# Optimization experiments

Hardware: AMD Instinct MI355X
Metric: run time of the kernel (lower is better)

## Reference

```python
import jax, jax.numpy as jnp
import numpy as np

N_HEAD, D_EMB, D_MLP, D_HEAD = 12, 768, 3072, 64
LN_EPS = 1e-5


def setup_inputs() -> dict:
    key = jax.random.key(0)
    ks = jax.random.split(key, 12)
    s = 0.02
    return {
        "x": jax.random.normal(ks[0], (2, 4096, D_EMB), dtype=jnp.float32),
        "ln1_g": jnp.ones((D_EMB,), jnp.float32),
        "ln1_b": jnp.zeros((D_EMB,), jnp.float32),
        "wqkv_w": jax.random.normal(ks[1], (D_EMB, 3 * D_EMB), jnp.float32) * s,
        "wo_w": jax.random.normal(ks[2], (D_EMB, D_EMB), jnp.float32) * s,
        "wo_b": jnp.zeros((D_EMB,), jnp.float32),
        "ln2_g": jnp.ones((D_EMB,), jnp.float32),
        "ln2_b": jnp.zeros((D_EMB,), jnp.float32),
        "w1_w": jax.random.normal(ks[3], (D_EMB, D_MLP), jnp.float32) * s,
        "w1_b": jnp.zeros((D_MLP,), jnp.float32),
        "w2_w": jax.random.normal(ks[4], (D_MLP, D_EMB), jnp.float32) * s,
        "w2_b": jnp.zeros((D_EMB,), jnp.float32),
    }


def _layernorm(x, g, b):
    mu = jnp.mean(x, axis=-1, keepdims=True)
    var = jnp.var(x, axis=-1, keepdims=True)
    return (x - mu) * jax.lax.rsqrt(var + LN_EPS) * g + b


def _attn(x, wqkv_w, wo_w, wo_b):
    B, T, d = x.shape
    qkv = x @ wqkv_w  # [B,T,3d]
    q, k, v = jnp.split(qkv, 3, axis=-1)
    q = q.reshape(B, T, N_HEAD, D_HEAD).transpose(0, 2, 1, 3)  # [B,H,T,dh]
    k = k.reshape(B, T, N_HEAD, D_HEAD).transpose(0, 2, 1, 3)
    v = v.reshape(B, T, N_HEAD, D_HEAD).transpose(0, 2, 1, 3)
    A = jnp.einsum('bhqd,bhkd->bhqk', q, k) / np.sqrt(D_HEAD).astype(np.float32)
    mask = jnp.tril(jnp.ones((T, T), dtype=bool))
    A = jnp.where(mask, A, -jnp.inf)
    A = jax.nn.softmax(A - jax.lax.stop_gradient(jnp.max(A, axis=-1, keepdims=True)), axis=-1)
    y = jnp.einsum('bhqk,bhkd->bhqd', A, v)  # [B,H,T,dh]
    y = y.transpose(0, 2, 1, 3).reshape(B, T, d)
    return y @ wo_w + wo_b


def _mlp(x, w1_w, w1_b, w2_w, w2_b):
    h = jax.nn.gelu(x @ w1_w + w1_b, approximate=False)
    return h @ w2_w + w2_b


def reference(x, ln1_g, ln1_b, wqkv_w, wo_w, wo_b, ln2_g, ln2_b, w1_w, w1_b, w2_w, w2_b):
    x = x + _attn(_layernorm(x, ln1_g, ln1_b), wqkv_w, wo_w, wo_b)
    x = x + _mlp(_layernorm(x, ln2_g, ln2_b), w1_w, w1_b, w2_w, w2_b)
    return x
```

## Files before the change

### kernel.cpp

```cpp
#include <hip/hip_runtime.h>

#define T_SEQ 4096
#define D_EMB 768
#define N_HEAD 12
#define D_HEAD 64
#define D_MLP 3072
#define NTOK 8192
#define QSCALE 0.18033688011112043f

typedef __bf16 v8bf __attribute__((ext_vector_type(8)));
typedef float v4f __attribute__((ext_vector_type(4)));
typedef short v4s __attribute__((ext_vector_type(4)));
typedef unsigned v2u __attribute__((ext_vector_type(2)));

template <int N> struct IC { static constexpr int value = N; };

__device__ __forceinline__ unsigned short f2bf(float f) {
    unsigned int u = __float_as_uint(f);
    unsigned int r = (u + 0x7fffu + ((u >> 16) & 1u)) >> 16;
    return (unsigned short)r;
}

__device__ __forceinline__ void g2lds16(const void* g, void* l) {
    __builtin_amdgcn_global_load_lds(
        (const __attribute__((address_space(1))) void*)g,
        (__attribute__((address_space(3))) void*)l, 16, 0, 0);
}

__device__ __forceinline__ float fastrcp(float x) {
#if __has_builtin(__builtin_amdgcn_rcpf)
    return __builtin_amdgcn_rcpf(x);
#else
    return 1.f / x;
#endif
}

__device__ __forceinline__ void pl32swap(unsigned& a, unsigned& b) {
#if __has_builtin(__builtin_amdgcn_permlane32_swap)
    v2u r = __builtin_amdgcn_permlane32_swap(a, b, false, false);
    a = r[0]; b = r[1];
#else
    asm volatile("v_permlane32_swap_b32 %0, %1" : "+v"(a), "+v"(b));
#endif
}
__device__ __forceinline__ void pl16swap(unsigned& a, unsigned& b) {
#if __has_builtin(__builtin_amdgcn_permlane16_swap)
    v2u r = __builtin_amdgcn_permlane16_swap(a, b, false, false);
    a = r[0]; b = r[1];
#else
    asm volatile("v_permlane16_swap_b32 %0, %1" : "+v"(a), "+v"(b));
#endif
}

__device__ __forceinline__ int sg(int r) { return (r ^ (r >> 2)) & 3; }

__global__ void tcast_kernel(const float* __restrict__ in, unsigned short* __restrict__ out,
                             int K, int N) {
    __shared__ float tile[32][33];
    int k0 = blockIdx.y * 32, n0 = blockIdx.x * 32;
    int tx = threadIdx.x, ty = threadIdx.y;
    for (int i = ty; i < 32; i += 8)
        tile[i][tx] = in[(size_t)(k0 + i) * N + n0 + tx];
    __syncthreads();
    for (int i = ty; i < 32; i += 8)
        out[(size_t)(n0 + i) * K + k0 + tx] = f2bf(tile[tx][i]);
}

__global__ void vtrans_kernel(const unsigned short* __restrict__ in,
                              unsigned short* __restrict__ out) {
    __shared__ unsigned short tile[32][33];
    size_t base = (size_t)blockIdx.z * T_SEQ * D_HEAD;
    int t0 = blockIdx.x * 32, d0 = blockIdx.y * 32;
    int tx = threadIdx.x, ty = threadIdx.y;
    for (int i = ty; i < 32; i += 8)
        tile[i][tx] = in[base + (size_t)(t0 + i) * D_HEAD + d0 + tx];
    __syncthreads();
    size_t tbase = base + (size_t)(t0 >> 6) * 4096 + (t0 & 32);
    for (int i = ty; i < 32; i += 8)
        out[tbase + (size_t)(d0 + i) * 64 + tx] = tile[tx][i];
}

__global__ __launch_bounds__(256) void ln_kernel(const float* __restrict__ x,
                                                 const float* __restrict__ g,
                                                 const float* __restrict__ bta,
                                                 unsigned short* __restrict__ out) {
    int row = blockIdx.x;
    const float* xr = x + (size_t)row * D_EMB;
    int tid = threadIdx.x;
    float v[3];
    float s = 0.f, s2 = 0.f;
#pragma unroll
    for (int i = 0; i < 3; i++) {
        v[i] = xr[tid + i * 256];
        s += v[i];
        s2 += v[i] * v[i];
    }
#pragma unroll
    for (int o = 1; o < 64; o <<= 1) {
        s += __shfl_xor(s, o);
        s2 += __shfl_xor(s2, o);
    }
    __shared__ float red[8];
    int wave = tid >> 6, lane = tid & 63;
    if (lane == 0) { red[wave] = s; red[wave + 4] = s2; }
    __syncthreads();
    s = red[0] + red[1] + red[2] + red[3];
    s2 = red[4] + red[5] + red[6] + red[7];
    float mu = s * (1.f / 768.f);
    float var = s2 * (1.f / 768.f) - mu * mu;
    float rstd = rsqrtf(var + 1e-5f);
#pragma unroll
    for (int i = 0; i < 3; i++) {
        int c = tid + i * 256;
        out[(size_t)row * D_EMB + c] = f2bf((v[i] - mu) * rstd * g[c] + bta[c]);
    }
}

template <int EPI, int MT>
__global__ __launch_bounds__(256) void gemm_kernel(
    const unsigned short* __restrict__ A, const unsigned short* __restrict__ Bt, int K,
    int Nt, const float* __restrict__ bias, const float* __restrict__ resid,
    float* __restrict__ outF, unsigned short* __restrict__ outB,
    unsigned short* __restrict__ Qb, unsigned short* __restrict__ Kb,
    unsigned short* __restrict__ Vb) {
    constexpr int NAI = (MT == 128) ? 4 : 2;
    __shared__ unsigned short As[2][MT * 32];
    __shared__ unsigned short Bs[2][4096];
    const int tid = threadIdx.x;
    const int wave = tid >> 6, lane = tid & 63;
    const int n16 = lane & 15, kq = lane >> 4;
    const int moff = (wave >> 1) * (MT / 2), noff = (wave & 1) * 64;
    const int id = blockIdx.x;
    const int xcd = id & 7, s = id >> 3;
    const int mt = xcd * (NTOK / MT / 8) + s / Nt, nt_ = s % Nt;
    const long m0 = (long)mt * MT, nb0 = (long)nt_ * 128;

    const int c0 = (wave * 2 + 0) * 64 + lane;
    const int c1 = (wave * 2 + 1) * 64 + lane;
    const int r0 = c0 >> 2, r1 = c1 >> 2;
    const unsigned short* bP0 = Bt + (nb0 + r0) * K + (((c0 & 3) ^ sg(r0)) << 3);
    const unsigned short* bP1 = Bt + (nb0 + r1) * K + (((c1 & 3) ^ sg(r1)) << 3);
    const int ca = (MT == 128) ? c0 : (wave * 64 + lane);
    const int ra = ca >> 2;
    const unsigned short* aP0 = A + (m0 + ra) * K + (((ca & 3) ^ sg(ra)) << 3);
    const unsigned short* aP1 = (MT == 128)
        ? A + (m0 + r1) * K + (((c1 & 3) ^ sg(r1)) << 3) : nullptr;
    const int sn = sg(n16);
    const int fw = (noff + n16) * 32 + ((kq ^ sn) << 3);
    const int fa = (moff + n16) * 32 + ((kq ^ sn) << 3);

    const v4f vzero = {0.f, 0.f, 0.f, 0.f};
    v4f acc[4][NAI];
#pragma unroll
    for (int wi = 0; wi < 4; wi++)
#pragma unroll
        for (int ai = 0; ai < NAI; ai++) acc[wi][ai] = vzero;

    auto stage = [&](auto BUFC, int kpos) {
        constexpr int nb = decltype(BUFC)::value;
        if (MT == 128) {
            g2lds16(aP0 + kpos, &As[nb][(wave * 2 + 0) * 512]);
            g2lds16(aP1 + kpos, &As[nb][(wave * 2 + 1) * 512]);
        } else {
            g2lds16(aP0 + kpos, &As[nb][wave * 512]);
        }
        g2lds16(bP0 + kpos, &Bs[nb][(wave * 2 + 0) * 512]);
        g2lds16(bP1 + kpos, &Bs[nb][(wave * 2 + 1) * 512]);
    };
    auto gstep = [&](auto BUFC, int kpos, bool pref) {
        constexpr int buf = decltype(BUFC)::value;
        __syncthreads();
        if (pref) stage(IC<buf ^ 1>{}, kpos + 32);
        v8bf wf[4], af[NAI];
#pragma unroll
        for (int i = 0; i < 4; i++) wf[i] = *(const v8bf*)(&Bs[buf][fw + i * 512]);
#pragma unroll
        for (int i = 0; i < NAI; i++) af[i] = *(const v8bf*)(&As[buf][fa + i * 512]);
#pragma unroll
        for (int wi = 0; wi < 4; wi++)
#pragma unroll
            for (int ai = 0; ai < NAI; ai++)
                acc[wi][ai] = __builtin_amdgcn_mfma_f32_16x16x32_bf16(wf[wi], af[ai],
                                                                     acc[wi][ai], 0, 0, 0);
    };

    stage(IC<0>{}, 0);
#pragma unroll 1
    for (int k0 = 0; k0 < K; k0 += 64) {
        gstep(IC<0>{}, k0, true);
        gstep(IC<1>{}, k0 + 32, k0 + 64 < K);
    }

#pragma unroll
    for (int wi = 0; wi < 4; wi++) {
#pragma unroll
        for (int ai = 0; ai < NAI; ai++) {
            const long Nb = nb0 + noff + wi * 16 + kq * 4;
            const long M = m0 + moff + ai * 16 + n16;
            if (EPI == 0) {
                int which = (int)(Nb / 768);
                int c = (int)(Nb - which * 768);
                int hh = c >> 6, ii = c & 63;
                int bb = (int)(M >> 12), t = (int)(M & 4095);
                size_t dst = (((size_t)bb * N_HEAD + hh) * T_SEQ + t) * D_HEAD + ii;
                union { uint2 u2; unsigned short us[4]; } pk;
#pragma unroll
                for (int r = 0; r < 4; r++) {
                    float v = acc[wi][ai][r];
                    if (which == 0) v *= QSCALE;
                    pk.us[r] = f2bf(v);
                }
                if (which == 0) *(uint2*)(&Qb[dst]) = pk.u2;
                else if (which == 1) *(uint2*)(&Kb[dst]) = pk.u2;
                else *(uint2*)(&Vb[dst]) = pk.u2;
            } else if (EPI == 1) {
                float4 b4 = *(const float4*)(&bias[Nb]);
                float4 r4 = *(const float4*)(&resid[M * 768 + Nb]);
                float4 o4;
                o4.x = acc[wi][ai][0] + b4.x + r4.x;
                o4.y = acc[wi][ai][1] + b4.y + r4.y;
                o4.z = acc[wi][ai][2] + b4.z + r4.z;
                o4.w = acc[wi][ai][3] + b4.w + r4.w;
                *(float4*)(&outF[M * 768 + Nb]) = o4;
            } else {
                float4 b4 = *(const float4*)(&bias[Nb]);
                union { uint2 u2; unsigned short us[4]; } pk;
#pragma unroll
                for (int r = 0; r < 4; r++) {
                    float t = acc[wi][ai][r] + ((const float*)&b4)[r];
                    float y = t * (-2.302118131f + t * t * -0.1029433585f);
                    float gl = t * fastrcp(1.f + __builtin_amdgcn_exp2f(y));
                    pk.us[r] = f2bf(gl);
                }
                *(uint2*)(&outB[M * 3072 + Nb]) = pk.u2;
            }
        }
    }
}

__global__ __launch_bounds__(256) void attn_kernel(const unsigned short* __restrict__ Q,
                                                   const unsigned short* __restrict__ Kg,
                                                   const unsigned short* __restrict__ Vt,
                                                   unsigned short* __restrict__ y) {
    __shared__ unsigned short Kt[2][4096];
    __shared__ unsigned short Vl[2][4096];
    const int tid = threadIdx.x;
    const int wave = tid >> 6, lane = tid & 63;
    const int n16 = lane & 15, kq = lane >> 4;
    const int id = blockIdx.x;
    const int xcd = id & 7, slot = id >> 3;
    const int combo = xcd * 3 + (slot % 3);
    const int qt = 63 - slot / 3;
    const int h = combo % N_HEAD, b = combo / N_HEAD;
    const size_t hoff = (((size_t)b * N_HEAD + h) * T_SEQ) * D_HEAD;
    const unsigned short* Qh = Q + hoff;
    const unsigned short* Kh = Kg + hoff;
    const unsigned short* Vh = Vt + hoff;
    const v4f vzero = {0.f, 0.f, 0.f, 0.f};

    const int sC0 = (wave * 2 + 0) * 64 + lane;
    const int sC1 = (wave * 2 + 1) * 64 + lane;
    const int soff0 = (sC0 >> 3) * 64 + ((((sC0 & 7) ^ ((sC0 >> 3) & 7))) << 3);
    const int soff1 = (sC1 >> 3) * 64 + ((((sC1 & 7) ^ ((sC1 >> 3) & 7))) << 3);
    const int fb0 = n16 * 64 + ((kq ^ (n16 & 7)) << 3);
    const int fb1 = n16 * 64 + (((4 + kq) ^ (n16 & 7)) << 3);
    v8bf vone;
#pragma unroll
    for (int j = 0; j < 8; j++) ((unsigned short*)&vone)[j] = 0x3F80;

    const int qglob = qt * 64 + wave * 16 + n16;
    v8bf qf[2];
#pragma unroll
    for (int ks = 0; ks < 2; ks++)
        qf[ks] = *(const v8bf*)(&Qh[(size_t)qglob * D_HEAD + ks * 32 + kq * 8]);

    v4f o[4], lacc;
#pragma unroll
    for (int nt = 0; nt < 4; nt++) o[nt] = vzero;
    lacc = vzero;

    const unsigned short* knext;
    const unsigned short* vnext;

    auto step = [&](auto BUFC, int kt, bool pref, bool diag) {
        constexpr int buf = decltype(BUFC)::value;
        __syncthreads();
        if (pref) {
            g2lds16(knext + soff0, &Kt[buf ^ 1][(wave * 2 + 0) * 512]);
            g2lds16(knext + soff1, &Kt[buf ^ 1][(wave * 2 + 1) * 512]);
            g2lds16(vnext + soff0, &Vl[buf ^ 1][(wave * 2 + 0) * 512]);
            g2lds16(vnext + soff1, &Vl[buf ^ 1][(wave * 2 + 1) * 512]);
            knext += 4096;
            vnext += 4096;
        }
        v4f s[4];
#pragma unroll
        for (int nt = 0; nt < 4; nt++) s[nt] = vzero;
        __builtin_amdgcn_s_setprio(1);
#pragma unroll
        for (int nt = 0; nt < 4; nt++) {
            v8bf k0 = *(const v8bf*)(&Kt[buf][nt * 1024 + fb0]);
            v8bf k1 = *(const v8bf*)(&Kt[buf][nt * 1024 + fb1]);
            s[nt] = __builtin_amdgcn_mfma_f32_16x16x32_bf16(k0, qf[0], s[nt], 0, 0, 0);
            s[nt] = __builtin_amdgcn_mfma_f32_16x16x32_bf16(k1, qf[1], s[nt], 0, 0, 0);
        }
        __builtin_amdgcn_s_setprio(0);
        union PW { v4s s4; unsigned u[2]; } pa[4];
#pragma unroll
        for (int ntk = 0; ntk < 4; ntk++) {
            union { v4s s4; __bf16 h[4]; } pk;
#pragma unroll
            for (int r = 0; r < 4; r++) {
                float p = __builtin_amdgcn_exp2f(s[ntk][r]);
                if (diag) {
                    int key = kt * 64 + ntk * 16 + kq * 4 + r;
                    if (key > qglob) p = 0.f;
                }
                pk.h[r] = (__bf16)p;
            }
            pa[ntk].s4 = pk.s4;
        }
        union F8 { v8bf v; unsigned u[4]; } pf[2];
#pragma unroll
        for (int ks = 0; ks < 2; ks++) {
#pragma unroll
            for (int j = 0; j < 2; j++) {
                unsigned X = pa[2 * ks].u[j], Y = pa[2 * ks + 1].u[j];
                pl32swap(X, Y);
                pl16swap(X, Y);
                pf[ks].u[j] = X;
                pf[ks].u[j + 2] = Y;
            }
        }
        __builtin_amdgcn_s_setprio(1);
#pragma unroll
        for (int ks = 0; ks < 2; ks++) {
            lacc = __builtin_amdgcn_mfma_f32_16x16x32_bf16(pf[ks].v, vone, lacc, 0, 0, 0);
#pragma unroll
            for (int nt = 0; nt < 4; nt++) {
                v8bf vb = *(const v8bf*)(&Vl[buf][nt * 1024 + (ks ? fb1 : fb0)]);
                o[nt] = __builtin_amdgcn_mfma_f32_16x16x32_bf16(pf[ks].v, vb, o[nt], 0, 0, 0);
            }
        }
        __builtin_amdgcn_s_setprio(0);
    };

    g2lds16(Kh + soff0, &Kt[0][(wave * 2 + 0) * 512]);
    g2lds16(Kh + soff1, &Kt[0][(wave * 2 + 1) * 512]);
    g2lds16(Vh + soff0, &Vl[0][(wave * 2 + 0) * 512]);
    g2lds16(Vh + soff1, &Vl[0][(wave * 2 + 1) * 512]);
    knext = Kh + 4096;
    vnext = Vh + 4096;

    int kt = 0;
#pragma unroll 1
    while (kt + 2 <= qt) {
        step(IC<0>{}, kt, true, false);
        step(IC<1>{}, kt + 1, true, false);
        kt += 2;
    }
    if (kt < qt) {
        step(IC<0>{}, kt, true, false);
        step(IC<1>{}, kt + 1, false, true);
    } else {
        step(IC<0>{}, kt, false, true);
    }

    float linv[4];
#pragma unroll
    for (int r = 0; r < 4; r++) linv[r] = fastrcp(lacc[r]);
#pragma unroll
    for (int nt = 0; nt < 4; nt++)
#pragma unroll
        for (int r = 0; r < 4; r++) {
            int q = qt * 64 + wave * 16 + kq * 4 + r;
            float val = o[nt][r] * linv[r];
            y[((size_t)b * T_SEQ + q) * D_EMB + h * 64 + nt * 16 + n16] = f2bf(val);
        }
}

extern "C" void kernel_launch(void* const* d_in, const int* in_sizes, int n_in,
                              void* d_out, int out_size, void* d_ws, size_t ws_size,
                              hipStream_t stream) {
    const float* x = (const float*)d_in[0];
    const float* ln1_g = (const float*)d_in[1];
    const float* ln1_b = (const float*)d_in[2];
    const float* wqkv_w = (const float*)d_in[3];
    const float* wo_w = (const float*)d_in[4];
    const float* wo_b = (const float*)d_in[5];
    const float* ln2_g = (const float*)d_in[6];
    const float* ln2_b = (const float*)d_in[7];
    const float* w1_w = (const float*)d_in[8];
    const float* w1_b = (const float*)d_in[9];
    const float* w2_w = (const float*)d_in[10];
    const float* w2_b = (const float*)d_in[11];
    float* out = (float*)d_out;

    char* ws = (char*)d_ws;
    size_t off = 0;
    auto alloc = [&](size_t bytes) -> void* {
        void* p = ws + off;
        off += (bytes + 255) & ~(size_t)255;
        return p;
    };
    unsigned short* xn = (unsigned short*)alloc((size_t)NTOK * D_EMB * 2);
    unsigned short* wqkvT = (unsigned short*)alloc((size_t)2304 * 768 * 2);
    unsigned short* woT = (unsigned short*)alloc((size_t)768 * 768 * 2);
    unsigned short* w1T = (unsigned short*)alloc((size_t)3072 * 768 * 2);
    unsigned short* w2T = (unsigned short*)alloc((size_t)768 * 3072 * 2);
    unsigned short* Qb = (unsigned short*)alloc((size_t)NTOK * D_EMB * 2);
    unsigned short* Kb = (unsigned short*)alloc((size_t)NTOK * D_EMB * 2);
    unsigned short* Vb = (unsigned short*)alloc((size_t)NTOK * D_EMB * 2);
    unsigned short* yb = (unsigned short*)alloc((size_t)NTOK * D_EMB * 2);
    float* res1 = (float*)alloc((size_t)NTOK * D_EMB * 4);
    unsigned short* Vtb = xn;
    unsigned short* hbuf = Qb;

    dim3 tb(32, 8);
    tcast_kernel<<<dim3(2304 / 32, 768 / 32), tb, 0, stream>>>(wqkv_w, wqkvT, 768, 2304);
    tcast_kernel<<<dim3(768 / 32, 768 / 32), tb, 0, stream>>>(wo_w, woT, 768, 768);
    tcast_kernel<<<dim3(3072 / 32, 768 / 32), tb, 0, stream>>>(w1_w, w1T, 768, 3072);
    tcast_kernel<<<dim3(768 / 32, 3072 / 32), tb, 0, stream>>>(w2_w, w2T, 3072, 768);

    ln_kernel<<<NTOK, 256, 0, stream>>>(x, ln1_g, ln1_b, xn);

    gemm_kernel<0, 128><<<1152, 256, 0, stream>>>(
        xn, wqkvT, 768, 18, nullptr, nullptr, nullptr, nullptr, Qb, Kb, Vb);

    vtrans_kernel<<<dim3(T_SEQ / 32, 2, 2 * N_HEAD), tb, 0, stream>>>(Vb, Vtb);

    attn_kernel<<<1536, 256, 0, stream>>>(Qb, Kb, Vtb, yb);

    gemm_kernel<1, 64><<<768, 256, 0, stream>>>(
        yb, woT, 768, 6, wo_b, x, res1, nullptr, nullptr, nullptr, nullptr);

    ln_kernel<<<NTOK, 256, 0, stream>>>(res1, ln2_g, ln2_b, xn);

    gemm_kernel<2, 128><<<1536, 256, 0, stream>>>(
        xn, w1T, 768, 24, w1_b, nullptr, nullptr, hbuf, nullptr, nullptr, nullptr);

    gemm_kernel<1, 64><<<768, 256, 0, stream>>>(
        hbuf, w2T, 3072, 6, w2_b, res1, out, nullptr, nullptr, nullptr, nullptr);
}
```

Baseline: 426.4 us.

## Triple-buffer GEMM LDS staging with explicit vmcnt waits

Moves the GEMM main loop from double-buffered LDS staging to a three-stage ring buffer. Loads for step i+2 are issued before computing step i. Partial s_waitcnt vmcnt counts plus a raw s_barrier replace the __syncthreads, so one step's global-to-LDS loads stay in flight across each barrier. This is meant to hide global memory latency better, at the cost of 50% more LDS per block, which may reduce occupancy, and with hand-counted waits that depend on the exact number of loads issued per stage.

```diff
diff --git a/kernel.cpp b/kernel.cpp
--- a/kernel.cpp
+++ b/kernel.cpp
@@ -124,8 +124,8 @@
     unsigned short* __restrict__ Qb, unsigned short* __restrict__ Kb,
     unsigned short* __restrict__ Vb) {
     constexpr int NAI = (MT == 128) ? 4 : 2;
-    __shared__ unsigned short As[2][MT * 32];
-    __shared__ unsigned short Bs[2][4096];
+    __shared__ unsigned short As[3][MT * 32];
+    __shared__ unsigned short Bs[3][4096];
     const int tid = threadIdx.x;
     const int wave = tid >> 6, lane = tid & 63;
     const int n16 = lane & 15, kq = lane >> 4;
@@ -156,26 +156,40 @@
 #pragma unroll
         for (int ai = 0; ai < NAI; ai++) acc[wi][ai] = vzero;
 
-    auto stage = [&](auto BUFC, int kpos) {
-        constexpr int nb = decltype(BUFC)::value;
+    auto stage = [&](int nb, int kpos) {
+        unsigned short* asb = &As[0][0] + nb * (MT * 32);
+        unsigned short* bsb = &Bs[0][0] + nb * 4096;
         if (MT == 128) {
-            g2lds16(aP0 + kpos, &As[nb][(wave * 2 + 0) * 512]);
-            g2lds16(aP1 + kpos, &As[nb][(wave * 2 + 1) * 512]);
+            g2lds16(aP0 + kpos, asb + (wave * 2 + 0) * 512);
+            g2lds16(aP1 + kpos, asb + (wave * 2 + 1) * 512);
         } else {
-            g2lds16(aP0 + kpos, &As[nb][wave * 512]);
-        }
-        g2lds16(bP0 + kpos, &Bs[nb][(wave * 2 + 0) * 512]);
-        g2lds16(bP1 + kpos, &Bs[nb][(wave * 2 + 1) * 512]);
-    };
-    auto gstep = [&](auto BUFC, int kpos, bool pref) {
-        constexpr int buf = decltype(BUFC)::value;
-        __syncthreads();
-        if (pref) stage(IC<buf ^ 1>{}, kpos + 32);
+            g2lds16(aP0 + kpos, asb + wave * 512);
+        }
+        g2lds16(bP0 + kpos, bsb + (wave * 2 + 0) * 512);
+        g2lds16(bP1 + kpos, bsb + (wave * 2 + 1) * 512);
+    };
+    auto waitL = [&]() {
+        if constexpr (MT == 128) {
+            asm volatile("s_waitcnt vmcnt(4)" ::: "memory");
+        } else {
+            asm volatile("s_waitcnt vmcnt(3)" ::: "memory");
+        }
+        __builtin_amdgcn_s_barrier();
+        __builtin_amdgcn_sched_barrier(0);
+    };
+    auto wait0 = [&]() {
+        asm volatile("s_waitcnt vmcnt(0)" ::: "memory");
+        __builtin_amdgcn_s_barrier();
+        __builtin_amdgcn_sched_barrier(0);
+    };
+    auto compute = [&](int nb) {
+        const unsigned short* asb = &As[0][0] + nb * (MT * 32);
+        const unsigned short* bsb = &Bs[0][0] + nb * 4096;
         v8bf wf[4], af[NAI];
 #pragma unroll
-        for (int i = 0; i < 4; i++) wf[i] = *(const v8bf*)(&Bs[buf][fw + i * 512]);
-#pragma unroll
-        for (int i = 0; i < NAI; i++) af[i] = *(const v8bf*)(&As[buf][fa + i * 512]);
+        for (int i = 0; i < 4; i++) wf[i] = *(const v8bf*)(bsb + fw + i * 512);
+#pragma unroll
+        for (int i = 0; i < NAI; i++) af[i] = *(const v8bf*)(asb + fa + i * 512);
 #pragma unroll
         for (int wi = 0; wi < 4; wi++)
 #pragma unroll
@@ -184,12 +198,23 @@
                                                                      acc[wi][ai], 0, 0, 0);
     };
 
-    stage(IC<0>{}, 0);
+    stage(0, 0);
+    stage(1, 32);
+    const int nsteps = K / 32;
+    int b0 = 0;
 #pragma unroll 1
-    for (int k0 = 0; k0 < K; k0 += 64) {
-        gstep(IC<0>{}, k0, true);
-        gstep(IC<1>{}, k0 + 32, k0 + 64 < K);
-    }
+    for (int i = 0; i < nsteps - 2; i++) {
+        waitL();
+        int b2 = b0 + 2; if (b2 >= 3) b2 -= 3;
+        stage(b2, (i + 2) * 32);
+        compute(b0);
+        b0++; if (b0 >= 3) b0 = 0;
+    }
+    waitL();
+    compute(b0);
+    b0++; if (b0 >= 3) b0 = 0;
+    wait0();
+    compute(b0);
 
 #pragma unroll
     for (int wi = 0; wi < 4; wi++) {
```

After: 424.7 us. No clear change (-0.4%).
